# Kernel optimization log

Measured on AMD Instinct MI355X. Metric: run time of the kernel, lower is better.

## Reference

```python
import jax, jax.numpy as jnp
import numpy as np

B = 256
N_SNP = 100000
BITS = 4          # snp_onehot_bits
BLOCK = 20        # SNPs per block
N_BLOCKS = N_SNP // BLOCK            # 5000 output blocks
IN_DIM = N_SNP * BITS                # 400000
DIMS = [1024, 256]
OUT_DIM = 1
LN_EPS = 1e-5


def _make_indices():
    # blocks_gt[i] = [20*i, ..., 20*i+19]; replicate get_param4sparse
    blocks = np.arange(N_SNP, dtype=np.int64).reshape(N_BLOCKS, BLOCK)
    idx0 = (blocks[:, :, None] * BITS + np.arange(BITS)).reshape(-1)   # input bit index, [nnz]
    idx1 = np.repeat(np.arange(N_BLOCKS, dtype=np.int64), BLOCK * BITS)  # output block index, [nnz]
    return jnp.asarray(idx0, jnp.int32), jnp.asarray(idx1, jnp.int32)


def setup_inputs() -> dict:
    key = jax.random.key(0)
    ks = jax.random.split(key, 9)
    idx0, idx1 = _make_indices()
    x = jax.random.uniform(ks[0], (B, IN_DIM), dtype=jnp.float32)
    sparse_values = jax.random.normal(ks[1], (idx0.shape[0],), dtype=jnp.float32)
    ln_gamma = jnp.ones((N_BLOCKS,), jnp.float32)
    ln_beta = jnp.zeros((N_BLOCKS,), jnp.float32)
    s1 = 1.0 / np.sqrt(N_BLOCKS)
    W1 = jax.random.uniform(ks[2], (DIMS[0], N_BLOCKS), jnp.float32, -s1, s1)
    b1 = jax.random.uniform(ks[3], (DIMS[0],), jnp.float32, -s1, s1)
    s2 = 1.0 / np.sqrt(DIMS[0])
    W2 = jax.random.uniform(ks[4], (DIMS[1], DIMS[0]), jnp.float32, -s2, s2)
    b2 = jax.random.uniform(ks[5], (DIMS[1],), jnp.float32, -s2, s2)
    s3 = 1.0 / np.sqrt(DIMS[1])
    W3 = jax.random.uniform(ks[6], (OUT_DIM, DIMS[1]), jnp.float32, -s3, s3)
    b3 = jax.random.uniform(ks[7], (OUT_DIM,), jnp.float32, -s3, s3)
    return {"x": x, "sparse_values": sparse_values, "ln_gamma": ln_gamma,
            "ln_beta": ln_beta, "W1": W1, "b1": b1, "W2": W2, "b2": b2,
            "W3": W3, "b3": b3, "idx0": idx0, "idx1": idx1}


def reference(x, sparse_values, ln_gamma, ln_beta, W1, b1, W2, b2, W3, b3, idx0, idx1):
    # SparseLinear: out[b, j] = sum_{k: idx1[k]==j} sparse_values[k] * x[b, idx0[k]]
    gathered = x[:, idx0] * sparse_values[None, :]                       # [B, nnz]
    gblocks = jax.ops.segment_sum(gathered.T, idx1, num_segments=N_BLOCKS).T  # [B, n_blocks]
    # LayerNorm over block dim
    mu = jnp.mean(gblocks, axis=-1, keepdims=True)
    var = jnp.mean(jnp.square(gblocks - mu), axis=-1, keepdims=True)
    h = (gblocks - mu) * jax.lax.rsqrt(var + LN_EPS) * ln_gamma + ln_beta
    # Dense head (note: no activation after first Linear, faithful to source)
    h = h @ W1.T + b1
    h = h @ W2.T + b2
    h = jax.nn.sigmoid(h)
    return h @ W3.T + b3                                                 # [B, OUT_DIM]
```

## Files before the change

### kernel.cpp

```cpp
#include <hip/hip_runtime.h>
#include <math.h>

#define BATCH   256
#define NBLK    5000
#define NBLKP   5024
#define IN_DIM  400000
#define D1      1024
#define D2      256
#define K1P     5120
#define NSPLIT  16
#define ZK      (K1P / NSPLIT)
#define ZSTEPS  (ZK / 64)

typedef __attribute__((ext_vector_type(8))) short short8_t;
typedef __attribute__((ext_vector_type(4))) float f32x4;

static __device__ __forceinline__ unsigned short f2bf(float f) {
    union { float f; unsigned int u; } v; v.f = f;
    unsigned int u = v.u;
    return (unsigned short)((u + 0x7FFFu + ((u >> 16) & 1u)) >> 16);
}

__global__ __launch_bounds__(256) void k_sparse(const float* __restrict__ x,
                                                const float* __restrict__ sv,
                                                float* __restrict__ g) {
    const int b   = blockIdx.y;
    const int tid = threadIdx.x;
    const int jj  = tid >> 2;
    const int s   = tid & 3;
    const int j   = blockIdx.x * 64 + jj;
    if (j >= NBLK) return;
    const float4* xr = reinterpret_cast<const float4*>(x + (size_t)b * IN_DIM + (size_t)j * 80);
    const float4* sr = reinterpret_cast<const float4*>(sv + (size_t)j * 80);
    float acc = 0.0f;
#pragma unroll
    for (int r = 0; r < 5; ++r) {
        float4 xv = xr[r * 4 + s];
        float4 sg = sr[r * 4 + s];
        acc += xv.x * sg.x + xv.y * sg.y + xv.z * sg.z + xv.w * sg.w;
    }
    acc += __shfl_xor(acc, 1);
    acc += __shfl_xor(acc, 2);
    if (s == 0) g[(size_t)b * NBLKP + j] = acc;
}

__global__ __launch_bounds__(256) void k_ln(const float* __restrict__ g,
                                            const float* __restrict__ gamma,
                                            const float* __restrict__ beta,
                                            unsigned short* __restrict__ A) {
    const int b   = blockIdx.x;
    const int tid = threadIdx.x;
    const float* row = g + (size_t)b * NBLKP;
    float v[20];
    float s = 0.0f, ss = 0.0f;
#pragma unroll
    for (int i = 0; i < 20; ++i) {
        const int j = tid + i * 256;
        const float xv = (j < NBLK) ? row[j] : 0.0f;
        v[i] = xv; s += xv; ss += xv * xv;
    }
#pragma unroll
    for (int o = 32; o > 0; o >>= 1) {
        s  += __shfl_xor(s, o);
        ss += __shfl_xor(ss, o);
    }
    __shared__ float ls[4], lss[4];
    const int wid = tid >> 6;
    if ((tid & 63) == 0) { ls[wid] = s; lss[wid] = ss; }
    __syncthreads();
    s  = ls[0] + ls[1] + ls[2] + ls[3];
    ss = lss[0] + lss[1] + lss[2] + lss[3];
    const float mu  = s / (float)NBLK;
    const float var = ss / (float)NBLK - mu * mu;
    const float rs  = rsqrtf(var + 1e-5f);
    unsigned short* dst = A + (size_t)b * K1P;
#pragma unroll
    for (int i = 0; i < 20; ++i) {
        const int j = tid + i * 256;
        const float val = (j < NBLK) ? ((v[i] - mu) * rs * gamma[j] + beta[j]) : 0.0f;
        dst[j] = f2bf(val);
    }
}

__global__ __launch_bounds__(256) void k_gemm1(const unsigned short* __restrict__ A,
                                               const float* __restrict__ W1,
                                               float* __restrict__ C) {
    const int n0 = blockIdx.x * 64;
    const int z  = blockIdx.y;
    const int kbase = z * ZK;
    float* Cz = C + (size_t)z * BATCH * D1;

    __shared__ unsigned short As[256][72];
    __shared__ unsigned short Ws[64][72];

    const int tid  = threadIdx.x;
    const int wave = tid >> 6;
    const int lane = tid & 63;
    const int lr   = lane & 15;
    const int lk   = (lane >> 4) * 8;
    const int srow = tid >> 3;
    const int scol = (tid & 7) * 8;
    const int wrow = tid >> 2;
    const int wcol = (tid & 3) * 16;

    const unsigned short* Ap = A + (size_t)srow * K1P + kbase + scol;
    const float* Wrow = W1 + (size_t)(n0 + wrow) * NBLK;

    short8_t pa[8];
    float4 pwf[4];
    auto loadA = [&](int t) {
#pragma unroll
        for (int it = 0; it < 8; ++it)
            pa[it] = *reinterpret_cast<const short8_t*>(Ap + (size_t)it * 32 * K1P + t * 64);
    };
    auto loadW = [&](int t) {
        const int k0 = kbase + t * 64 + wcol;
#pragma unroll
        for (int q = 0; q < 4; ++q) {
            const int k = k0 + q * 4;
            pwf[q] = (k < NBLK) ? *reinterpret_cast<const float4*>(Wrow + k)
                                : float4{0.f, 0.f, 0.f, 0.f};
        }
    };

    loadA(0);
    loadW(0);

    f32x4 acc[4][4] = {};

    for (int t = 0; t < ZSTEPS; ++t) {
        __syncthreads();
#pragma unroll
        for (int it = 0; it < 8; ++it)
            *reinterpret_cast<short8_t*>(&As[srow + it * 32][scol]) = pa[it];
        {
            short8_t w0 = { (short)f2bf(pwf[0].x), (short)f2bf(pwf[0].y), (short)f2bf(pwf[0].z), (short)f2bf(pwf[0].w),
                            (short)f2bf(pwf[1].x), (short)f2bf(pwf[1].y), (short)f2bf(pwf[1].z), (short)f2bf(pwf[1].w) };
            short8_t w1 = { (short)f2bf(pwf[2].x), (short)f2bf(pwf[2].y), (short)f2bf(pwf[2].z), (short)f2bf(pwf[2].w),
                            (short)f2bf(pwf[3].x), (short)f2bf(pwf[3].y), (short)f2bf(pwf[3].z), (short)f2bf(pwf[3].w) };
            *reinterpret_cast<short8_t*>(&Ws[wrow][wcol])     = w0;
            *reinterpret_cast<short8_t*>(&Ws[wrow][wcol + 8]) = w1;
        }
        __syncthreads();
        if (t + 1 < ZSTEPS) { loadA(t + 1); loadW(t + 1); }
#pragma unroll
        for (int kk = 0; kk < 64; kk += 32) {
            short8_t a[4], b[4];
#pragma unroll
            for (int i = 0; i < 4; ++i)
                a[i] = *reinterpret_cast<const short8_t*>(&As[wave * 64 + i * 16 + lr][kk + lk]);
#pragma unroll
            for (int j = 0; j < 4; ++j)
                b[j] = *reinterpret_cast<const short8_t*>(&Ws[j * 16 + lr][kk + lk]);
#pragma unroll
            for (int i = 0; i < 4; ++i)
#pragma unroll
                for (int j = 0; j < 4; ++j)
                    acc[i][j] = __builtin_amdgcn_mfma_f32_16x16x32_bf16(a[i], b[j], acc[i][j], 0, 0, 0);
        }
    }

    const int rbase = (lane >> 4) * 4;
#pragma unroll
    for (int i = 0; i < 4; ++i)
#pragma unroll
        for (int j = 0; j < 4; ++j) {
            const int col = n0 + j * 16 + lr;
#pragma unroll
            for (int r = 0; r < 4; ++r) {
                const int row = wave * 64 + i * 16 + rbase + r;
                Cz[(size_t)row * D1 + col] = acc[i][j][r];
            }
        }
}

__global__ __launch_bounds__(256) void k_fuse(const float* __restrict__ p,
                                              const float* __restrict__ b1,
                                              unsigned short* __restrict__ A2,
                                              const float* __restrict__ W2,
                                              unsigned short* __restrict__ W2b) {
    const int idx = (blockIdx.x * 256 + threadIdx.x) * 4;
    const int col = idx & (D1 - 1);
    const size_t S = (size_t)BATCH * D1;
    float4 bb = *reinterpret_cast<const float4*>(b1 + col);
    float sx = bb.x, sy = bb.y, sz = bb.z, sw = bb.w;
#pragma unroll
    for (int q = 0; q < NSPLIT; ++q) {
        float4 v = *reinterpret_cast<const float4*>(p + q * S + idx);
        sx += v.x; sy += v.y; sz += v.z; sw += v.w;
    }
    ushort4 o = { f2bf(sx), f2bf(sy), f2bf(sz), f2bf(sw) };
    *reinterpret_cast<ushort4*>(A2 + idx) = o;
    float4 wv = *reinterpret_cast<const float4*>(W2 + idx);
    ushort4 wo = { f2bf(wv.x), f2bf(wv.y), f2bf(wv.z), f2bf(wv.w) };
    *reinterpret_cast<ushort4*>(W2b + idx) = wo;
}

__global__ __launch_bounds__(512) void k_tail(const unsigned short* __restrict__ A2,
                                              const unsigned short* __restrict__ W2b,
                                              const float* __restrict__ b2,
                                              const float* __restrict__ W3,
                                              const float* __restrict__ b3,
                                              float* __restrict__ out) {
    const int m0 = blockIdx.x * 32;
    __shared__ unsigned short As[32][72];
    __shared__ unsigned short Ws[256][72];
    __shared__ float red[8][32];

    const int tid  = threadIdx.x;
    const int wave = tid >> 6;
    const int lane = tid & 63;
    const int wc   = wave * 32;
    const int lr   = lane & 15;
    const int lk   = (lane >> 4) * 8;
    const int srow = tid >> 3;
    const int scol = (tid & 7) * 8;

    const unsigned short* Ap = A2 + (size_t)(m0 + srow) * D1 + scol;
    const unsigned short* Wp = W2b + (size_t)srow * D1 + scol;

    short8_t pa = {};
    short8_t pw[4];
    if (tid < 256) pa = *reinterpret_cast<const short8_t*>(Ap);
#pragma unroll
    for (int it = 0; it < 4; ++it)
        pw[it] = *reinterpret_cast<const short8_t*>(Wp + (size_t)it * 64 * D1);

    f32x4 acc[2][2] = {};

    for (int t = 0; t < 16; ++t) {
        __syncthreads();
        if (tid < 256) *reinterpret_cast<short8_t*>(&As[srow][scol]) = pa;
#pragma unroll
        for (int it = 0; it < 4; ++it)
            *reinterpret_cast<short8_t*>(&Ws[srow + it * 64][scol]) = pw[it];
        __syncthreads();
        if (t + 1 < 16) {
            const int ko = (t + 1) * 64;
            if (tid < 256) pa = *reinterpret_cast<const short8_t*>(Ap + ko);
#pragma unroll
            for (int it = 0; it < 4; ++it)
                pw[it] = *reinterpret_cast<const short8_t*>(Wp + (size_t)it * 64 * D1 + ko);
        }
#pragma unroll
        for (int kk = 0; kk < 64; kk += 32) {
            short8_t a0 = *reinterpret_cast<const short8_t*>(&As[lr][kk + lk]);
            short8_t a1 = *reinterpret_cast<const short8_t*>(&As[16 + lr][kk + lk]);
#pragma unroll
            for (int j = 0; j < 2; ++j) {
                short8_t bj = *reinterpret_cast<const short8_t*>(&Ws[wc + j * 16 + lr][kk + lk]);
                acc[0][j] = __builtin_amdgcn_mfma_f32_16x16x32_bf16(a0, bj, acc[0][j], 0, 0, 0);
                acc[1][j] = __builtin_amdgcn_mfma_f32_16x16x32_bf16(a1, bj, acc[1][j], 0, 0, 0);
            }
        }
    }

    float b2c[2], w3c[2];
#pragma unroll
    for (int j = 0; j < 2; ++j) {
        const int col = wc + j * 16 + lr;
        b2c[j] = b2[col];
        w3c[j] = W3[col];
    }
    const int rbase = (lane >> 4) * 4;
#pragma unroll
    for (int i = 0; i < 2; ++i) {
#pragma unroll
        for (int r = 0; r < 4; ++r) {
            float pv = 0.0f;
#pragma unroll
            for (int j = 0; j < 2; ++j) {
                const float h = acc[i][j][r] + b2c[j];
                pv += w3c[j] / (1.0f + __expf(-h));
            }
            pv += __shfl_xor(pv, 1);
            pv += __shfl_xor(pv, 2);
            pv += __shfl_xor(pv, 4);
            pv += __shfl_xor(pv, 8);
            if (lr == 0) red[wave][i * 16 + rbase + r] = pv;
        }
    }
    __syncthreads();
    if (tid < 32) {
        float s2 = 0.0f;
#pragma unroll
        for (int w = 0; w < 8; ++w) s2 += red[w][tid];
        out[m0 + tid] = s2 + b3[0];
    }
}

extern "C" void kernel_launch(void* const* d_in, const int* in_sizes, int n_in,
                              void* d_out, int out_size, void* d_ws, size_t ws_size,
                              hipStream_t stream) {
    const float* x     = (const float*)d_in[0];
    const float* sv    = (const float*)d_in[1];
    const float* gamma = (const float*)d_in[2];
    const float* beta  = (const float*)d_in[3];
    const float* W1    = (const float*)d_in[4];
    const float* b1    = (const float*)d_in[5];
    const float* W2    = (const float*)d_in[6];
    const float* b2    = (const float*)d_in[7];
    const float* W3    = (const float*)d_in[8];
    const float* b3    = (const float*)d_in[9];
    float* out = (float*)d_out;

    char* ws = (char*)d_ws;
    size_t off = 0;
    auto alloc = [&](size_t bytes) { char* p = ws + off; off = (off + bytes + 255) & ~(size_t)255; return p; };
    float*          g     = (float*)         alloc((size_t)BATCH * NBLKP * 4);
    unsigned short* Ab    = (unsigned short*)alloc((size_t)BATCH * K1P * 2);
    float*          out1p = (float*)         alloc((size_t)NSPLIT * BATCH * D1 * 4);
    unsigned short* A2b   = (unsigned short*)alloc((size_t)BATCH * D1 * 2);
    unsigned short* W2b   = (unsigned short*)alloc((size_t)D2 * D1 * 2);

    k_sparse<<<dim3((NBLK + 63) / 64, BATCH), 256, 0, stream>>>(x, sv, g);
    k_ln<<<dim3(BATCH), 256, 0, stream>>>(g, gamma, beta, Ab);
    k_gemm1<<<dim3(D1 / 64, NSPLIT), 256, 0, stream>>>(Ab, W1, out1p);
    k_fuse<<<dim3(BATCH * D1 / (256 * 4)), 256, 0, stream>>>(out1p, b1, A2b, W2, W2b);
    k_tail<<<dim3(BATCH / 32), 512, 0, stream>>>(A2b, W2b, b2, W3, b3, out);
}
```

Baseline: 128.8 us.

## Fuse sparse+LayerNorm, retile GEMM1 split, fold split-K reduce into tail

Merges the sparse block-sum and LayerNorm into one 1024-thread kernel per batch row, keeping the block sums in shared memory so the intermediate global buffer and one launch disappear. GEMM1 now uses 32-column tiles and 8 K-splits instead of 64-column tiles and 16, which halves the split-K partial traffic while keeping the grid at 256 workgroups. The separate split-K reduce and W2 conversion kernel is removed. The tail kernel now sums the partials, converts W2 to bf16 on the fly and processes 8 rows per block (padded to 16 for MFMA). That gives the tail more blocks, but half of each MFMA is wasted and W2 is reconverted in every block.

```diff
diff --git a/kernel.cpp b/kernel.cpp
--- a/kernel.cpp
+++ b/kernel.cpp
@@ -3,12 +3,11 @@
 
 #define BATCH   256
 #define NBLK    5000
-#define NBLKP   5024
 #define IN_DIM  400000
 #define D1      1024
 #define D2      256
 #define K1P     5120
-#define NSPLIT  16
+#define NSPLIT  8
 #define ZK      (K1P / NSPLIT)
 #define ZSTEPS  (ZK / 64)
 
@@ -21,77 +20,104 @@
     return (unsigned short)((u + 0x7FFFu + ((u >> 16) & 1u)) >> 16);
 }
 
-__global__ __launch_bounds__(256) void k_sparse(const float* __restrict__ x,
-                                                const float* __restrict__ sv,
-                                                float* __restrict__ g) {
-    const int b   = blockIdx.y;
-    const int tid = threadIdx.x;
-    const int jj  = tid >> 2;
-    const int s   = tid & 3;
-    const int j   = blockIdx.x * 64 + jj;
-    if (j >= NBLK) return;
-    const float4* xr = reinterpret_cast<const float4*>(x + (size_t)b * IN_DIM + (size_t)j * 80);
-    const float4* sr = reinterpret_cast<const float4*>(sv + (size_t)j * 80);
-    float acc = 0.0f;
-#pragma unroll
-    for (int r = 0; r < 5; ++r) {
-        float4 xv = xr[r * 4 + s];
-        float4 sg = sr[r * 4 + s];
-        acc += xv.x * sg.x + xv.y * sg.y + xv.z * sg.z + xv.w * sg.w;
-    }
-    acc += __shfl_xor(acc, 1);
-    acc += __shfl_xor(acc, 2);
-    if (s == 0) g[(size_t)b * NBLKP + j] = acc;
-}
-
-__global__ __launch_bounds__(256) void k_ln(const float* __restrict__ g,
-                                            const float* __restrict__ gamma,
-                                            const float* __restrict__ beta,
-                                            unsigned short* __restrict__ A) {
+__global__ __launch_bounds__(1024) void k_sparse_ln(const float* __restrict__ x,
+                                                    const float* __restrict__ sv,
+                                                    const float* __restrict__ gamma,
+                                                    const float* __restrict__ beta,
+                                                    unsigned short* __restrict__ A) {
+    __shared__ float gbuf[NBLK];
+    __shared__ float ls[16], lss[16];
     const int b   = blockIdx.x;
     const int tid = threadIdx.x;
-    const float* row = g + (size_t)b * NBLKP;
-    float v[20];
-    float s = 0.0f, ss = 0.0f;
-#pragma unroll
-    for (int i = 0; i < 20; ++i) {
-        const int j = tid + i * 256;
-        const float xv = (j < NBLK) ? row[j] : 0.0f;
-        v[i] = xv; s += xv; ss += xv * xv;
+    const int grp = tid >> 2;
+    const int s   = tid & 3;
+    const float* xb = x + (size_t)b * IN_DIM;
+
+#pragma unroll
+    for (int i = 0; i < 20; i += 2) {
+        const int j0 = grp + i * 256;
+        const int j1 = grp + (i + 1) * 256;
+        const bool v1 = (j1 < NBLK);
+        const float4* xr0 = reinterpret_cast<const float4*>(xb + (size_t)j0 * 80);
+        const float4* sr0 = reinterpret_cast<const float4*>(sv + (size_t)j0 * 80);
+        const float4* xr1 = reinterpret_cast<const float4*>(xb + (size_t)j1 * 80);
+        const float4* sr1 = reinterpret_cast<const float4*>(sv + (size_t)j1 * 80);
+        float4 xa[5], sa[5], xc[5], sc[5];
+#pragma unroll
+        for (int r = 0; r < 5; ++r) { xa[r] = xr0[r * 4 + s]; sa[r] = sr0[r * 4 + s]; }
+        if (v1) {
+#pragma unroll
+            for (int r = 0; r < 5; ++r) { xc[r] = xr1[r * 4 + s]; sc[r] = sr1[r * 4 + s]; }
+        }
+        float a0 = 0.f, a1 = 0.f;
+#pragma unroll
+        for (int r = 0; r < 5; ++r)
+            a0 += xa[r].x * sa[r].x + xa[r].y * sa[r].y + xa[r].z * sa[r].z + xa[r].w * sa[r].w;
+        if (v1) {
+#pragma unroll
+            for (int r = 0; r < 5; ++r)
+                a1 += xc[r].x * sc[r].x + xc[r].y * sc[r].y + xc[r].z * sc[r].z + xc[r].w * sc[r].w;
+        }
+        a0 += __shfl_xor(a0, 1); a0 += __shfl_xor(a0, 2);
+        a1 += __shfl_xor(a1, 1); a1 += __shfl_xor(a1, 2);
+        if (s == 0) {
+            gbuf[j0] = a0;
+            if (v1) gbuf[j1] = a1;
+        }
+    }
+    __syncthreads();
+
+    float sm = 0.f, ssm = 0.f;
+    for (int j = tid; j < NBLK; j += 1024) {
+        const float v = gbuf[j];
+        sm += v; ssm += v * v;
     }
 #pragma unroll
     for (int o = 32; o > 0; o >>= 1) {
-        s  += __shfl_xor(s, o);
-        ss += __shfl_xor(ss, o);
-    }
-    __shared__ float ls[4], lss[4];
-    const int wid = tid >> 6;
-    if ((tid & 63) == 0) { ls[wid] = s; lss[wid] = ss; }
+        sm  += __shfl_xor(sm, o);
+        ssm += __shfl_xor(ssm, o);
+    }
+    if ((tid & 63) == 0) { ls[tid >> 6] = sm; lss[tid >> 6] = ssm; }
     __syncthreads();
-    s  = ls[0] + ls[1] + ls[2] + ls[3];
-    ss = lss[0] + lss[1] + lss[2] + lss[3];
-    const float mu  = s / (float)NBLK;
-    const float var = ss / (float)NBLK - mu * mu;
+    float S = 0.f, SS = 0.f;
+#pragma unroll
+    for (int w = 0; w < 16; ++w) { S += ls[w]; SS += lss[w]; }
+    const float mu  = S / (float)NBLK;
+    const float var = SS / (float)NBLK - mu * mu;
     const float rs  = rsqrtf(var + 1e-5f);
+
     unsigned short* dst = A + (size_t)b * K1P;
 #pragma unroll
-    for (int i = 0; i < 20; ++i) {
-        const int j = tid + i * 256;
-        const float val = (j < NBLK) ? ((v[i] - mu) * rs * gamma[j] + beta[j]) : 0.0f;
-        dst[j] = f2bf(val);
+    for (int p = 0; p < 2; ++p) {
+        const int jj = p * 4096 + tid * 4;
+        if (jj < K1P) {
+            ushort4 o;
+            if (jj < NBLK) {
+                float4 gv = *reinterpret_cast<const float4*>(&gbuf[jj]);
+                float4 gm = *reinterpret_cast<const float4*>(gamma + jj);
+                float4 bt = *reinterpret_cast<const float4*>(beta + jj);
+                o = { f2bf((gv.x - mu) * rs * gm.x + bt.x),
+                      f2bf((gv.y - mu) * rs * gm.y + bt.y),
+                      f2bf((gv.z - mu) * rs * gm.z + bt.z),
+                      f2bf((gv.w - mu) * rs * gm.w + bt.w) };
+            } else {
+                o = ushort4{0, 0, 0, 0};
+            }
+            *reinterpret_cast<ushort4*>(dst + jj) = o;
+        }
     }
 }
 
 __global__ __launch_bounds__(256) void k_gemm1(const unsigned short* __restrict__ A,
                                                const float* __restrict__ W1,
                                                float* __restrict__ C) {
-    const int n0 = blockIdx.x * 64;
+    const int n0 = blockIdx.x * 32;
     const int z  = blockIdx.y;
     const int kbase = z * ZK;
     float* Cz = C + (size_t)z * BATCH * D1;
 
     __shared__ unsigned short As[256][72];
-    __shared__ unsigned short Ws[64][72];
+    __shared__ unsigned short Ws[32][72];
 
     const int tid  = threadIdx.x;
     const int wave = tid >> 6;
@@ -100,14 +126,14 @@
     const int lk   = (lane >> 4) * 8;
     const int srow = tid >> 3;
     const int scol = (tid & 7) * 8;
-    const int wrow = tid >> 2;
-    const int wcol = (tid & 3) * 16;
+    const int wrow = tid >> 3;
+    const int wcol = (tid & 7) * 8;
 
     const unsigned short* Ap = A + (size_t)srow * K1P + kbase + scol;
     const float* Wrow = W1 + (size_t)(n0 + wrow) * NBLK;
 
     short8_t pa[8];
-    float4 pwf[4];
+    float4 pwf[2];
     auto loadA = [&](int t) {
 #pragma unroll
         for (int it = 0; it < 8; ++it)
@@ -116,7 +142,7 @@
     auto loadW = [&](int t) {
         const int k0 = kbase + t * 64 + wcol;
 #pragma unroll
-        for (int q = 0; q < 4; ++q) {
+        for (int q = 0; q < 2; ++q) {
             const int k = k0 + q * 4;
             pwf[q] = (k < NBLK) ? *reinterpret_cast<const float4*>(Wrow + k)
                                 : float4{0.f, 0.f, 0.f, 0.f};
@@ -126,7 +152,7 @@
     loadA(0);
     loadW(0);
 
-    f32x4 acc[4][4] = {};
+    f32x4 acc[4][2] = {};
 
     for (int t = 0; t < ZSTEPS; ++t) {
         __syncthreads();
@@ -136,27 +162,24 @@
         {
             short8_t w0 = { (short)f2bf(pwf[0].x), (short)f2bf(pwf[0].y), (short)f2bf(pwf[0].z), (short)f2bf(pwf[0].w),
                             (short)f2bf(pwf[1].x), (short)f2bf(pwf[1].y), (short)f2bf(pwf[1].z), (short)f2bf(pwf[1].w) };
-            short8_t w1 = { (short)f2bf(pwf[2].x), (short)f2bf(pwf[2].y), (short)f2bf(pwf[2].z), (short)f2bf(pwf[2].w),
-                            (short)f2bf(pwf[3].x), (short)f2bf(pwf[3].y), (short)f2bf(pwf[3].z), (short)f2bf(pwf[3].w) };
-            *reinterpret_cast<short8_t*>(&Ws[wrow][wcol])     = w0;
-            *reinterpret_cast<short8_t*>(&Ws[wrow][wcol + 8]) = w1;
+            *reinterpret_cast<short8_t*>(&Ws[wrow][wcol]) = w0;
         }
         __syncthreads();
         if (t + 1 < ZSTEPS) { loadA(t + 1); loadW(t + 1); }
 #pragma unroll
         for (int kk = 0; kk < 64; kk += 32) {
-            short8_t a[4], b[4];
+            short8_t a[4], bfr[2];
 #pragma unroll
             for (int i = 0; i < 4; ++i)
                 a[i] = *reinterpret_cast<const short8_t*>(&As[wave * 64 + i * 16 + lr][kk + lk]);
 #pragma unroll
-            for (int j = 0; j < 4; ++j)
-                b[j] = *reinterpret_cast<const short8_t*>(&Ws[j * 16 + lr][kk + lk]);
+            for (int j = 0; j < 2; ++j)
+                bfr[j] = *reinterpret_cast<const short8_t*>(&Ws[j * 16 + lr][kk + lk]);
 #pragma unroll
             for (int i = 0; i < 4; ++i)
 #pragma unroll
-                for (int j = 0; j < 4; ++j)
-                    acc[i][j] = __builtin_amdgcn_mfma_f32_16x16x32_bf16(a[i], b[j], acc[i][j], 0, 0, 0);
+                for (int j = 0; j < 2; ++j)
+                    acc[i][j] = __builtin_amdgcn_mfma_f32_16x16x32_bf16(a[i], bfr[j], acc[i][j], 0, 0, 0);
         }
     }
 
@@ -164,7 +187,7 @@
 #pragma unroll
     for (int i = 0; i < 4; ++i)
 #pragma unroll
-        for (int j = 0; j < 4; ++j) {
+        for (int j = 0; j < 2; ++j) {
             const int col = n0 + j * 16 + lr;
 #pragma unroll
             for (int r = 0; r < 4; ++r) {
@@ -174,38 +197,17 @@
         }
 }
 
-__global__ __launch_bounds__(256) void k_fuse(const float* __restrict__ p,
+__global__ __launch_bounds__(512) void k_tail(const float* __restrict__ p,
                                               const float* __restrict__ b1,
-                                              unsigned short* __restrict__ A2,
                                               const float* __restrict__ W2,
-                                              unsigned short* __restrict__ W2b) {
-    const int idx = (blockIdx.x * 256 + threadIdx.x) * 4;
-    const int col = idx & (D1 - 1);
-    const size_t S = (size_t)BATCH * D1;
-    float4 bb = *reinterpret_cast<const float4*>(b1 + col);
-    float sx = bb.x, sy = bb.y, sz = bb.z, sw = bb.w;
-#pragma unroll
-    for (int q = 0; q < NSPLIT; ++q) {
-        float4 v = *reinterpret_cast<const float4*>(p + q * S + idx);
-        sx += v.x; sy += v.y; sz += v.z; sw += v.w;
-    }
-    ushort4 o = { f2bf(sx), f2bf(sy), f2bf(sz), f2bf(sw) };
-    *reinterpret_cast<ushort4*>(A2 + idx) = o;
-    float4 wv = *reinterpret_cast<const float4*>(W2 + idx);
-    ushort4 wo = { f2bf(wv.x), f2bf(wv.y), f2bf(wv.z), f2bf(wv.w) };
-    *reinterpret_cast<ushort4*>(W2b + idx) = wo;
-}
-
-__global__ __launch_bounds__(512) void k_tail(const unsigned short* __restrict__ A2,
-                                              const unsigned short* __restrict__ W2b,
                                               const float* __restrict__ b2,
                                               const float* __restrict__ W3,
                                               const float* __restrict__ b3,
                                               float* __restrict__ out) {
-    const int m0 = blockIdx.x * 32;
-    __shared__ unsigned short As[32][72];
-    __shared__ unsigned short Ws[256][72];
-    __shared__ float red[8][32];
+    const int m0 = blockIdx.x * 8;
+    __shared__ unsigned short As2[16][1032];
+    __shared__ unsigned short Ws2[256][72];
+    __shared__ float red[8][16];
 
     const int tid  = threadIdx.x;
     const int wave = tid >> 6;
@@ -213,46 +215,57 @@
     const int wc   = wave * 32;
     const int lr   = lane & 15;
     const int lk   = (lane >> 4) * 8;
-    const int srow = tid >> 3;
-    const int scol = (tid & 7) * 8;
-
-    const unsigned short* Ap = A2 + (size_t)(m0 + srow) * D1 + scol;
-    const unsigned short* Wp = W2b + (size_t)srow * D1 + scol;
-
-    short8_t pa = {};
-    short8_t pw[4];
-    if (tid < 256) pa = *reinterpret_cast<const short8_t*>(Ap);
-#pragma unroll
-    for (int it = 0; it < 4; ++it)
-        pw[it] = *reinterpret_cast<const short8_t*>(Wp + (size_t)it * 64 * D1);
-
-    f32x4 acc[2][2] = {};
-
+
+    const int wrow  = tid >> 1;
+    const int wcolh = (tid & 1) * 32;
+    const float* Wbase = W2 + (size_t)wrow * D1 + wcolh;
+    float4 pw[8];
+    auto loadW = [&](int t) {
+#pragma unroll
+        for (int q = 0; q < 8; ++q)
+            pw[q] = *reinterpret_cast<const float4*>(Wbase + t * 64 + q * 4);
+    };
+    loadW(0);
+
+    const size_t S = (size_t)BATCH * D1;
+#pragma unroll
+    for (int sl = 0; sl < 4; ++sl) {
+        const int flat = sl * 2048 + tid * 4;
+        const int row  = flat >> 10;
+        const int col  = flat & 1023;
+        const float* base = p + (size_t)(m0 + row) * D1 + col;
+        float4 a = *reinterpret_cast<const float4*>(b1 + col);
+#pragma unroll
+        for (int q = 0; q < NSPLIT; ++q) {
+            float4 v = *reinterpret_cast<const float4*>(base + q * S);
+            a.x += v.x; a.y += v.y; a.z += v.z; a.w += v.w;
+        }
+        ushort4 o = { f2bf(a.x), f2bf(a.y), f2bf(a.z), f2bf(a.w) };
+        *reinterpret_cast<ushort4*>(&As2[row][col]) = o;
+        *reinterpret_cast<ushort4*>(&As2[row + 8][col]) = ushort4{0, 0, 0, 0};
+    }
+    __syncthreads();
+
+    f32x4 acc[2] = {};
     for (int t = 0; t < 16; ++t) {
+#pragma unroll
+        for (int q2 = 0; q2 < 4; ++q2) {
+            short8_t w = { (short)f2bf(pw[2*q2].x), (short)f2bf(pw[2*q2].y), (short)f2bf(pw[2*q2].z), (short)f2bf(pw[2*q2].w),
+                           (short)f2bf(pw[2*q2+1].x), (short)f2bf(pw[2*q2+1].y), (short)f2bf(pw[2*q2+1].z), (short)f2bf(pw[2*q2+1].w) };
+            *reinterpret_cast<short8_t*>(&Ws2[wrow][wcolh + q2 * 8]) = w;
+        }
         __syncthreads();
-        if (tid < 256) *reinterpret_cast<short8_t*>(&As[srow][scol]) = pa;
-#pragma unroll
-        for (int it = 0; it < 4; ++it)
-            *reinterpret_cast<short8_t*>(&Ws[srow + it * 64][scol]) = pw[it];
+        if (t + 1 < 16) loadW(t + 1);
+#pragma unroll
+        for (int kk = 0; kk < 64; kk += 32) {
+            short8_t a = *reinterpret_cast<const short8_t*>(&As2[lr][t * 64 + kk + lk]);
+#pragma unroll
+            for (int j = 0; j < 2; ++j) {
+                short8_t bb = *reinterpret_cast<const short8_t*>(&Ws2[wc + j * 16 + lr][kk + lk]);
+                acc[j] = __builtin_amdgcn_mfma_f32_16x16x32_bf16(a, bb, acc[j], 0, 0, 0);
+            }
+        }
         __syncthreads();
-        if (t + 1 < 16) {
-            const int ko = (t + 1) * 64;
-            if (tid < 256) pa = *reinterpret_cast<const short8_t*>(Ap + ko);
-#pragma unroll
-            for (int it = 0; it < 4; ++it)
-                pw[it] = *reinterpret_cast<const short8_t*>(Wp + (size_t)it * 64 * D1 + ko);
-        }
-#pragma unroll
-        for (int kk = 0; kk < 64; kk += 32) {
-            short8_t a0 = *reinterpret_cast<const short8_t*>(&As[lr][kk + lk]);
-            short8_t a1 = *reinterpret_cast<const short8_t*>(&As[16 + lr][kk + lk]);
-#pragma unroll
-            for (int j = 0; j < 2; ++j) {
-                short8_t bj = *reinterpret_cast<const short8_t*>(&Ws[wc + j * 16 + lr][kk + lk]);
-                acc[0][j] = __builtin_amdgcn_mfma_f32_16x16x32_bf16(a0, bj, acc[0][j], 0, 0, 0);
-                acc[1][j] = __builtin_amdgcn_mfma_f32_16x16x32_bf16(a1, bj, acc[1][j], 0, 0, 0);
-            }
-        }
     }
 
     float b2c[2], w3c[2];
@@ -264,24 +277,21 @@
     }
     const int rbase = (lane >> 4) * 4;
 #pragma unroll
-    for (int i = 0; i < 2; ++i) {
-#pragma unroll
-        for (int r = 0; r < 4; ++r) {
-            float pv = 0.0f;
-#pragma unroll
-            for (int j = 0; j < 2; ++j) {
-                const float h = acc[i][j][r] + b2c[j];
-                pv += w3c[j] / (1.0f + __expf(-h));
-            }
-            pv += __shfl_xor(pv, 1);
-            pv += __shfl_xor(pv, 2);
-            pv += __shfl_xor(pv, 4);
-            pv += __shfl_xor(pv, 8);
-            if (lr == 0) red[wave][i * 16 + rbase + r] = pv;
-        }
+    for (int r = 0; r < 4; ++r) {
+        float pv = 0.0f;
+#pragma unroll
+        for (int j = 0; j < 2; ++j) {
+            const float h = acc[j][r] + b2c[j];
+            pv += w3c[j] / (1.0f + __expf(-h));
+        }
+        pv += __shfl_xor(pv, 1);
+        pv += __shfl_xor(pv, 2);
+        pv += __shfl_xor(pv, 4);
+        pv += __shfl_xor(pv, 8);
+        if (lr == 0) red[wave][rbase + r] = pv;
     }
     __syncthreads();
-    if (tid < 32) {
+    if (tid < 8) {
         float s2 = 0.0f;
 #pragma unroll
         for (int w = 0; w < 8; ++w) s2 += red[w][tid];
@@ -307,15 +317,10 @@
     char* ws = (char*)d_ws;
     size_t off = 0;
     auto alloc = [&](size_t bytes) { char* p = ws + off; off = (off + bytes + 255) & ~(size_t)255; return p; };
-    float*          g     = (float*)         alloc((size_t)BATCH * NBLKP * 4);
     unsigned short* Ab    = (unsigned short*)alloc((size_t)BATCH * K1P * 2);
     float*          out1p = (float*)         alloc((size_t)NSPLIT * BATCH * D1 * 4);
-    unsigned short* A2b   = (unsigned short*)alloc((size_t)BATCH * D1 * 2);
-    unsigned short* W2b   = (unsigned short*)alloc((size_t)D2 * D1 * 2);
-
-    k_sparse<<<dim3((NBLK + 63) / 64, BATCH), 256, 0, stream>>>(x, sv, g);
-    k_ln<<<dim3(BATCH), 256, 0, stream>>>(g, gamma, beta, Ab);
-    k_gemm1<<<dim3(D1 / 64, NSPLIT), 256, 0, stream>>>(Ab, W1, out1p);
-    k_fuse<<<dim3(BATCH * D1 / (256 * 4)), 256, 0, stream>>>(out1p, b1, A2b, W2, W2b);
-    k_tail<<<dim3(BATCH / 32), 512, 0, stream>>>(A2b, W2b, b2, W3, b3, out);
-}
+
+    k_sparse_ln<<<dim3(BATCH), 1024, 0, stream>>>(x, sv, gamma, beta, Ab);
+    k_gemm1<<<dim3(D1 / 32, NSPLIT), 256, 0, stream>>>(Ab, W1, out1p);
+    k_tail<<<dim3(BATCH / 8), 512, 0, stream>>>(out1p, b1, W2, b2, W3, b3, out);
+}
```

Measured after the change: 162.1 us. 25.8% more time.
